# Kernel tuning notes

Hardware: AMD Instinct MI355X
Metric: run time of the kernel (lower is better)

## Reference

```python
import math
import jax, jax.numpy as jnp
import numpy as np

D_MODEL = 1024
N_HEAD = 16
HEAD_DIM = D_MODEL // N_HEAD  # 64
B = 8
L = 512
USE_GAUSSIAN = True
SCALE = 1.0  # scale=False in __init__


def rel_sin_pos_embed(seq_len, dim):
    # RelativeSinusoidalPositionalEmbedding: table row at index (pos+origin_shift)
    # holds [sin(pos*inv_freq), cos(pos*inv_freq)]; forward selects positions
    # arange(-L/2, round(L/2)) -> for even L this is -L/2 .. L/2-1.
    half = dim // 2
    inv_freq = jnp.exp(jnp.arange(half, dtype=jnp.float32) * (-math.log(10000.0) / (half - 1)))
    rel = jnp.arange(-(seq_len // 2), seq_len - seq_len // 2, dtype=jnp.float32)  # [L]
    ang = rel[:, None] * inv_freq[None, :]  # [L, half]
    return jnp.concatenate([jnp.sin(ang), jnp.cos(ang)], axis=-1)  # [L, dim]


def setup_inputs() -> dict:
    key = jax.random.key(0)
    ks = jax.random.split(key, 8)
    x = jax.random.normal(ks[0], (B, L, D_MODEL), dtype=jnp.float32)
    mask = jax.random.randint(ks[1], (B, L), 0, 2, dtype=jnp.int32)
    # guarantee at least one valid key per row so softmax never sees all -inf
    mask = mask.at[:, 0].set(1)
    qmask = jax.random.randint(ks[2], (B, L), 0, 2, dtype=jnp.int64)
    s = 0.02
    W_qkv = jax.random.normal(ks[3], (5 * D_MODEL, D_MODEL), dtype=jnp.float32) * s
    W_pos = jax.random.normal(ks[4], (3 * D_MODEL, HEAD_DIM), dtype=jnp.float32) * s
    W_fc = jax.random.normal(ks[5], (D_MODEL, D_MODEL), dtype=jnp.float32) * s
    b_fc = jnp.zeros((D_MODEL,), dtype=jnp.float32)
    # shift = abs(randn)+eps (positive), bias = -abs(randn); small scale keeps softmax sane
    shift = jnp.abs(jax.random.normal(ks[6], (1,), dtype=jnp.float32)) * 1e-4 + 1e-5
    bias = -jnp.abs(jax.random.normal(ks[7], (1,), dtype=jnp.float32))
    return {"x": x, "mask": mask, "qmask": qmask, "W_qkv": W_qkv, "W_pos": W_pos,
            "W_fc": W_fc, "b_fc": b_fc, "shift": shift, "bias": bias}


def reference(x, mask, qmask, W_qkv, W_pos, W_fc, b_fc, shift, bias):
    Bs, Ls, D = x.shape
    H, hd = N_HEAD, D // N_HEAD

    qkv = jnp.einsum('bld,ed->ble', x, W_qkv)  # [B, L, 5D]
    q, k, k1, k2, v = jnp.split(qkv, 5, axis=-1)

    def heads(t):  # [B, L, D] -> [B, H, L, hd]
        return t.reshape(Bs, Ls, H, hd).transpose(0, 2, 1, 3)

    q, k1, k2, v = heads(q), heads(k1), heads(k2), heads(v)

    pe = jax.lax.stop_gradient(rel_sin_pos_embed(Ls, hd))  # [L, hd], detached in torch
    y = jnp.einsum('ld,ed->le', pe, W_pos)  # [L, 3D]
    q_p, k1_p, k2_p = jnp.split(y, 3, axis=-1)
    q_p = q_p.reshape(Ls, H, hd).transpose(1, 0, 2)   # [H, L, hd]
    k1_p = k1_p.reshape(Ls, H, hd).transpose(1, 0, 2)  # [H, L, hd]
    k2_p = k2_p.reshape(Ls, H, hd).transpose(1, 0, 2)

    attn_self = jnp.einsum('bhid,bhjd->bhij', q, k1) + jnp.einsum('hid,hjd->hij', q_p, k1_p)[None]
    attn_others = jnp.einsum('bhid,bhjd->bhij', q, k2) + jnp.einsum('hid,hjd->hij', q_p, k2_p)[None]

    same = (qmask[:, :, None] == qmask[:, None, :])[:, None]  # [B, 1, L, L]
    attn = jnp.where(same, attn_self, 0.0) + jnp.where(same, 0.0, attn_others)
    attn = attn / SCALE
    attn = jnp.where(mask[:, None, None, :] == 0, -jnp.inf, attn)

    if USE_GAUSSIAN:
        idx = jnp.arange(Ls, dtype=jnp.float32)
        sq_dist = (idx[:, None] - idx[None, :]) ** 2  # [L, L]
        attn = attn + (-(shift[0] * sq_dist + bias[0]))[None, None]

    attn = jax.nn.softmax(attn, axis=-1)
    out = jnp.einsum('bhij,bhjd->bhid', attn, v)  # [B, H, L, hd]
    out = out.transpose(0, 2, 1, 3).reshape(Bs, Ls, D)
    return jnp.einsum('bld,ed->ble', out, W_fc) + b_fc
```

## Files before the change

### kernel.cpp

```cpp
#include <hip/hip_runtime.h>

#define DM 1024
#define HN 16
#define HD 64
#define BB 8
#define LL 512

typedef __bf16 bf16x8 __attribute__((ext_vector_type(8)));
typedef __bf16 bf16x4 __attribute__((ext_vector_type(4)));
typedef float  f32x4  __attribute__((ext_vector_type(4)));

__device__ __forceinline__ void cvt8(const float* __restrict__ in,
                                     __bf16* __restrict__ out, int i) {
    const float4* p = (const float4*)in + (size_t)i * 2;
    float4 a = p[0], b = p[1];
    bf16x8 v;
    v[0] = (__bf16)a.x; v[1] = (__bf16)a.y; v[2] = (__bf16)a.z; v[3] = (__bf16)a.w;
    v[4] = (__bf16)b.x; v[5] = (__bf16)b.y; v[6] = (__bf16)b.z; v[7] = (__bf16)b.w;
    ((bf16x8*)out)[i] = v;
}

__global__ __launch_bounds__(512) void prep_kernel(
    const int* __restrict__ qmask, const int* __restrict__ maskp,
    const float* __restrict__ x, const float* __restrict__ W_qkv,
    const float* __restrict__ W_pos, const float* __restrict__ W_fc,
    int* __restrict__ perm, int* __restrict__ pmask, float* __restrict__ posf,
    int* __restrict__ nzA, __bf16* __restrict__ PEb, __bf16* __restrict__ Wposb,
    __bf16* __restrict__ Wfcb, __bf16* __restrict__ Xb, __bf16* __restrict__ Wqkvb)
{
    const int blk = blockIdx.x, tid = threadIdx.x;
    if (blk < 8) {
        int b = blk, i = tid;
        int qm = qmask[b * LL + i];
        unsigned long long bz = __ballot(qm == 0);
        int wid = i >> 6, lane = i & 63;
        __shared__ int wz[8];
        int pzw = __popcll(bz & ((1ULL << lane) - 1ULL));
        if (lane == 0) wz[wid] = __popcll(bz);
        __syncthreads();
        int base = 0, nz = 0;
#pragma unroll
        for (int w2 = 0; w2 < 8; ++w2) { int c = wz[w2]; if (w2 < wid) base += c; nz += c; }
        int zbefore = base + pzw;
        int pos = (qm == 0) ? zbefore : (nz + (i - zbefore));
        perm[b * LL + pos] = i;
        pmask[b * LL + pos] = maskp[b * LL + i];
        posf[b * LL + pos] = (float)i;
        if (i == 0) nzA[b] = nz;
    } else if (blk < 72) {
        int idx = (blk - 8) * 512 + tid;
        int l = idx >> 6, d = idx & 63;
        float p = (float)(l - LL / 2);
        const float cexp = -9.210340371976184f / 31.0f;
        float val;
        if (d < 32) { float f = expf((float)d * cexp);        val = sinf(p * f); }
        else        { float f = expf((float)(d - 32) * cexp); val = cosf(p * f); }
        PEb[idx] = (__bf16)val;
    } else if (blk < 120) {
        cvt8(W_pos, Wposb, (blk - 72) * 512 + tid);
    } else if (blk < 376) {
        cvt8(W_fc, Wfcb, (blk - 120) * 512 + tid);
    } else if (blk < 1400) {
        cvt8(x, Xb, (blk - 376) * 512 + tid);
    } else if (blk < 1656) {
        cvt8(W_qkv, Wqkvb, (blk - 1400) * 512 + tid);
    } else {
        cvt8(W_qkv + 2097152, Wqkvb + 1048576, (blk - 1656) * 512 + tid);
    }
}

template<int MODE>
__global__ __launch_bounds__(256, 4) void gemm_mfma(
    const __bf16* __restrict__ A, const __bf16* __restrict__ Bm,
    __bf16* __restrict__ Qc, __bf16* __restrict__ K1c,
    __bf16* __restrict__ K2c, __bf16* __restrict__ Vn,
    float* __restrict__ outF, const float* __restrict__ bias, int K)
{
    __shared__ __bf16 smem[128 * 136];
    __bf16* As = smem;
    __bf16* Bs = smem + 8192;
    __bf16* Cs = smem;
    const int tid = threadIdx.x;
    const int lane = tid & 63;
    const int w = tid >> 6;
    const int wm = w >> 1, wn = w & 1;
    const int n0 = blockIdx.x * 128;
    const int m0 = blockIdx.y * 128;
    const int fr = lane & 15;
    const int fq = lane >> 4;

    const int srow = tid >> 3;
    const int scol = (tid & 7) ^ (srow & 7);
    const __bf16* Ag = A + (size_t)(m0 + srow) * K + scol * 8;
    const __bf16* Bg = Bm + (size_t)(n0 + srow) * K + scol * 8;
    char* AsB = (char*)As + (size_t)w * 1024;
    char* BsB = (char*)Bs + (size_t)w * 1024;

    f32x4 acc[4][4] = {};

    for (int k0 = 0; k0 < K; k0 += 64) {
#pragma unroll
        for (int r = 0; r < 4; ++r) {
            __builtin_amdgcn_global_load_lds(Ag + k0 + (size_t)(r * 32) * K, AsB + r * 4096, 16, 0, 0);
            __builtin_amdgcn_global_load_lds(Bg + k0 + (size_t)(r * 32) * K, BsB + r * 4096, 16, 0, 0);
        }
        __syncthreads();

#pragma unroll
        for (int kk = 0; kk < 2; ++kk) {
            const int so = ((kk * 4 + fq) ^ (fr & 7)) * 8;
            bf16x8 af[4], bfr[4];
#pragma unroll
            for (int i = 0; i < 4; ++i)
                af[i] = *(const bf16x8*)(As + (size_t)(wm * 64 + i * 16 + fr) * 64 + so);
#pragma unroll
            for (int j = 0; j < 4; ++j)
                bfr[j] = *(const bf16x8*)(Bs + (size_t)(wn * 64 + j * 16 + fr) * 64 + so);
#pragma unroll
            for (int i = 0; i < 4; ++i)
#pragma unroll
                for (int j = 0; j < 4; ++j)
                    acc[i][j] = __builtin_amdgcn_mfma_f32_16x16x32_bf16(bfr[j], af[i], acc[i][j], 0, 0, 0);
        }
        __syncthreads();
    }

    if constexpr (MODE == 0 || MODE == 2) {
#pragma unroll
        for (int i = 0; i < 4; ++i) {
            int mloc = wm * 64 + i * 16 + fr;
#pragma unroll
            for (int j = 0; j < 4; ++j) {
                int nloc = wn * 64 + j * 16 + fq * 4;
                bf16x4 v;
#pragma unroll
                for (int r = 0; r < 4; ++r) v[r] = (__bf16)acc[i][j][r];
                *(bf16x4*)(Cs + (size_t)mloc * 136 + nloc) = v;
            }
        }
        __syncthreads();
        if constexpr (MODE == 0) {
            const int c = n0 >> 10;
            __bf16* T = (c == 0) ? Qc : (c == 1) ? K1c : (c == 2) ? K2c : Vn;
            const int b = m0 >> 9, l0 = m0 & 511, h0 = (n0 >> 6) & 15;
#pragma unroll
            for (int rnd = 0; rnd < 8; ++rnd) {
                int Ci = rnd * 256 + tid;
                int m = Ci >> 4, nch = Ci & 15;
                bf16x8 v = *(const bf16x8*)(Cs + (size_t)m * 136 + nch * 8);
                int hl = nch >> 3, d = (nch & 7) * 8;
                size_t bh2 = (size_t)(b * HN + h0 + hl);
                if (c < 3) *(bf16x8*)(T + (bh2 * LL + l0 + m) * 128 + d) = v;
                else       *(bf16x8*)(T + (bh2 * LL + l0 + m) * 64  + d) = v;
            }
        } else {
            const int c = n0 >> 10;
            __bf16* T = (c == 0) ? Qc : (c == 1) ? K1c : K2c;
#pragma unroll
            for (int rnd = 0; rnd < 8; ++rnd) {
                int Ci = rnd * 256 + tid;
                int m = Ci >> 4, nch = Ci & 15;
                bf16x8 v = *(const bf16x8*)(Cs + (size_t)m * 136 + nch * 8);
                int eg = n0 + nch * 8;
                int h = (eg >> 6) & 15, d = eg & 63;
                size_t off = ((size_t)h * LL + (m0 + m)) * 128 + 64 + d;
#pragma unroll
                for (int b = 0; b < 8; ++b)
                    *(bf16x8*)(T + (size_t)b * (HN * LL * 128) + off) = v;
            }
        }
    } else {
#pragma unroll
        for (int i = 0; i < 4; ++i) {
            int m = m0 + wm * 64 + i * 16 + fr;
#pragma unroll
            for (int j = 0; j < 4; ++j) {
                int nn = n0 + wn * 64 + j * 16 + fq * 4;
                float4 bv = *(const float4*)(bias + nn);
                *(float4*)(outF + (size_t)m * DM + nn) =
                    make_float4(acc[i][j][0] + bv.x, acc[i][j][1] + bv.y,
                                acc[i][j][2] + bv.z, acc[i][j][3] + bv.w);
            }
        }
    }
}

__global__ __launch_bounds__(256) void vtrans_kernel(const __bf16* __restrict__ Vn,
                                                     const int* __restrict__ perm,
                                                     __bf16* __restrict__ Vt) {
    __shared__ __bf16 Ts[64][72];
    int bh = blockIdx.x >> 3, lt = blockIdx.x & 7;
    int b = bh >> 4;
    int r = threadIdx.x >> 2, s = threadIdx.x & 3;
    int orow = perm[b * LL + lt * 64 + r];
    const __bf16* src = Vn + ((size_t)bh * LL + orow) * 64;
    *(bf16x8*)&Ts[r][s * 16]     = *(const bf16x8*)(src + s * 16);
    *(bf16x8*)&Ts[r][s * 16 + 8] = *(const bf16x8*)(src + s * 16 + 8);
    __syncthreads();
    __bf16* dst = Vt + ((size_t)bh * 64 + r) * LL + lt * 64 + s * 16;
    bf16x8 a, bvv;
#pragma unroll
    for (int e = 0; e < 8; ++e) { a[e] = Ts[s * 16 + e][r]; bvv[e] = Ts[s * 16 + 8 + e][r]; }
    *(bf16x8*)dst = a;
    *(bf16x8*)(dst + 8) = bvv;
}

__global__ __launch_bounds__(512, 2) void attn_kernel(
    const __bf16* __restrict__ Qc, const __bf16* __restrict__ K1c,
    const __bf16* __restrict__ K2c, const __bf16* __restrict__ Vt,
    const int* __restrict__ pmask, const int* __restrict__ perm,
    const float* __restrict__ posf, const int* __restrict__ nzA,
    const float* __restrict__ shiftp, const float* __restrict__ biasp,
    __bf16* __restrict__ AO)
{
    __shared__ __bf16 Ke[2][64 * 128];
    __shared__ __bf16 Vts[64 * 72];
    __shared__ __bf16 Sb[8 * 16 * 40];
    __shared__ __align__(16) float posL[64];

    const int tid = threadIdx.x;
    const int lane = tid & 63;
    const int wid = tid >> 6;
    const int fr = lane & 15;
    const int fq = lane >> 4;
    const int fx = fr & 7;

    const int bid = (blockIdx.x & 7) * 64 + (blockIdx.x >> 3);
    const int qt = bid & 3;
    const int h  = (bid >> 2) & 15;
    const int b  = bid >> 6;
    const size_t bh = (size_t)(b * HN + h);
    const int nz = nzA[b];
    const int q0blk = qt * 128;
    const int s = q0blk + wid * 16 + fr;
    const int pi = perm[b * LL + s];
    const bool need0 = (q0blk < nz);
    const bool need1 = (q0blk + 127 >= nz);
    const int w0 = q0blk + wid * 16;
    const bool wneed0 = (w0 < nz);
    const bool wneed1 = (w0 + 15 >= nz);
    const int qmI = (s >= nz) ? 1 : 0;

    const float sft = shiftp[0];

    int co[4];
#pragma unroll
    for (int kf = 0; kf < 4; ++kf) co[kf] = ((kf * 4 + fq) ^ fx) * 8;

    bf16x8 qf[4];
    {
        const __bf16* qrow = Qc + (bh * LL + pi) * 128;
#pragma unroll
        for (int kf = 0; kf < 4; ++kf)
            qf[kf] = *(const bf16x8*)(qrow + kf * 32 + fq * 8);
    }

    float mrun = -1e30f, lrun = 0.f;
    f32x4 ot[4] = {};
    const float qposf = (float)pi;

    const __bf16* K1g0 = K1c + bh * LL * 128;
    const __bf16* K2g0 = K2c + bh * LL * 128;
    const __bf16* Vtg0 = Vt + bh * 64 * LL;
    __bf16* Sw = Sb + wid * 16 * 40;

    const int krr = tid >> 4;
    const int ku  = tid & 15;
    const int vrr = tid >> 3;
    const int vu  = tid & 7;

    bf16x8 rk0[2], rk1[2], rv;
    int pm; float ppos;

#define LOAD_TILE(tt)                                                              \
    {                                                                              \
        int j0_ = (tt) * 64;                                                       \
        _Pragma("unroll")                                                          \
        for (int p = 0; p < 2; ++p) {                                              \
            int sr = j0_ + p * 32 + krr;                                           \
            int orow = perm[b * LL + sr];                                          \
            int qmj = (sr >= nz) ? 1 : 0;                                          \
            const __bf16* s1 = (qmj ? K2g0 : K1g0) + (size_t)orow * 128 + ku * 8;  \
            const __bf16* s2 = (qmj ? K1g0 : K2g0) + (size_t)orow * 128 + ku * 8;  \
            if (need0) rk0[p] = *(const bf16x8*)s1;                                \
            if (need1) rk1[p] = *(const bf16x8*)s2;                                \
        }                                                                          \
        rv = *(const bf16x8*)(Vtg0 + (size_t)vrr * LL + j0_ + vu * 8);             \
        pm = pmask[b * LL + j0_ + lane];                                           \
        ppos = posf[b * LL + j0_ + lane];                                          \
    }

    LOAD_TILE(0);

    for (int t = 0; t < 8; ++t) {
        __syncthreads();
        {
#pragma unroll
            for (int p = 0; p < 2; ++p) {
                int rr = p * 32 + krr;
                int sc = (ku ^ (rr & 7)) * 8;
                if (need0) *(bf16x8*)(Ke[0] + rr * 128 + sc) = rk0[p];
                if (need1) *(bf16x8*)(Ke[1] + rr * 128 + sc) = rk1[p];
            }
            *(bf16x8*)(Vts + vrr * 72 + vu * 8) = rv;
            if (wid == 0) posL[lane] = ppos;
        }
        unsigned long long kbits = __ballot(pm != 0);
        if (t < 7) LOAD_TILE(t + 1);
        __syncthreads();

        f32x4 acc[4];
        if (wneed0 != wneed1) {
            const __bf16* Ks = wneed0 ? Ke[0] : Ke[1];
            __builtin_amdgcn_s_setprio(1);
#pragma unroll
            for (int kb = 0; kb < 4; ++kb) {
                const __bf16* row = Ks + (kb * 16 + fr) * 128;
                bf16x8 af[4];
#pragma unroll
                for (int kf = 0; kf < 4; ++kf)
                    af[kf] = *(const bf16x8*)(row + co[kf]);
                f32x4 a = {};
#pragma unroll
                for (int kf = 0; kf < 4; ++kf)
                    a = __builtin_amdgcn_mfma_f32_16x16x32_bf16(af[kf], qf[kf], a, 0, 0, 0);
                acc[kb] = a;
            }
            __builtin_amdgcn_s_setprio(0);
        } else {
            __builtin_amdgcn_s_setprio(1);
#pragma unroll
            for (int kb = 0; kb < 4; ++kb) {
                const __bf16* r0 = Ke[0] + (kb * 16 + fr) * 128;
                const __bf16* r1 = Ke[1] + (kb * 16 + fr) * 128;
                bf16x8 a0f[4], a1f[4];
#pragma unroll
                for (int kf = 0; kf < 4; ++kf) {
                    a0f[kf] = *(const bf16x8*)(r0 + co[kf]);
                    a1f[kf] = *(const bf16x8*)(r1 + co[kf]);
                }
                f32x4 t0 = {}, t1 = {};
#pragma unroll
                for (int kf = 0; kf < 4; ++kf) {
                    t0 = __builtin_amdgcn_mfma_f32_16x16x32_bf16(a0f[kf], qf[kf], t0, 0, 0, 0);
                    t1 = __builtin_amdgcn_mfma_f32_16x16x32_bf16(a1f[kf], qf[kf], t1, 0, 0, 0);
                }
#pragma unroll
                for (int r = 0; r < 4; ++r) acc[kb][r] = qmI ? t1[r] : t0[r];
            }
            __builtin_amdgcn_s_setprio(0);
        }

#pragma unroll
        for (int kb = 0; kb < 4; ++kb) {
            f32x4 pj = *(const f32x4*)(posL + kb * 16 + fq * 4);
#pragma unroll
            for (int r = 0; r < 4; ++r) {
                float di = qposf - pj[r];
                acc[kb][r] -= sft * di * di;
            }
        }

        float lmax = acc[0][0];
#pragma unroll
        for (int kb = 0; kb < 4; ++kb)
#pragma unroll
            for (int r = 0; r < 4; ++r) lmax = fmaxf(lmax, acc[kb][r]);
        if (!__all(lmax <= mrun + 8.f)) {
            float mn = fmaxf(mrun, lmax);
            mn = fmaxf(mn, __shfl_xor(mn, 16));
            mn = fmaxf(mn, __shfl_xor(mn, 32));
            float sc = __expf(mrun - mn);
            mrun = mn;
            lrun *= sc;
#pragma unroll
            for (int fd = 0; fd < 4; ++fd)
#pragma unroll
                for (int r = 0; r < 4; ++r) ot[fd][r] *= sc;
        }
        float sum = 0.f;
#pragma unroll
        for (int kb = 0; kb < 4; ++kb)
#pragma unroll
            for (int r = 0; r < 4; ++r) {
                int ko = kb * 16 + fq * 4 + r;
                float p = ((int)(kbits >> ko) & 1) ? __expf(acc[kb][r] - mrun) : 0.f;
                acc[kb][r] = p;
                sum += p;
            }
        sum += __shfl_xor(sum, 16);
        sum += __shfl_xor(sum, 32);
        lrun += sum;

        __builtin_amdgcn_s_setprio(1);
#pragma unroll
        for (int half = 0; half < 2; ++half) {
#pragma unroll
            for (int kk = 0; kk < 2; ++kk) {
                int kb = half * 2 + kk;
                bf16x4 pk;
#pragma unroll
                for (int r = 0; r < 4; ++r) pk[r] = (__bf16)acc[kb][r];
                *(bf16x4*)(Sw + fr * 40 + kk * 16 + fq * 4) = pk;
            }
            bf16x8 pf = *(const bf16x8*)(Sw + fr * 40 + fq * 8);
#pragma unroll
            for (int fd = 0; fd < 4; ++fd) {
                bf16x8 vf = *(const bf16x8*)(Vts + (fd * 16 + fr) * 72 + half * 32 + fq * 8);
                ot[fd] = __builtin_amdgcn_mfma_f32_16x16x32_bf16(vf, pf, ot[fd], 0, 0, 0);
            }
        }
        __builtin_amdgcn_s_setprio(0);
    }
#undef LOAD_TILE

    __syncthreads();
    {
        const float inv = 1.0f / lrun;
        __bf16* Ew = Ke[0] + (size_t)(wid * 16) * 72;
#pragma unroll
        for (int fd = 0; fd < 4; ++fd) {
            bf16x4 o;
#pragma unroll
            for (int r = 0; r < 4; ++r) o[r] = (__bf16)(ot[fd][r] * inv);
            *(bf16x4*)(Ew + fr * 72 + fd * 16 + fq * 4) = o;
        }
    }
    __syncthreads();
    {
        int r = tid >> 2, c = tid & 3;
        int pir = perm[b * LL + q0blk + r];
        const __bf16* src = Ke[0] + (size_t)r * 72;
        __bf16* dst = AO + ((size_t)(b * LL + pir)) * DM + h * 64;
        *(bf16x8*)(dst + c * 8)      = *(const bf16x8*)(src + c * 8);
        *(bf16x8*)(dst + 32 + c * 8) = *(const bf16x8*)(src + 32 + c * 8);
    }
}

extern "C" void kernel_launch(void* const* d_in, const int* in_sizes, int n_in,
                              void* d_out, int out_size, void* d_ws, size_t ws_size,
                              hipStream_t stream) {
    const float* x     = (const float*)d_in[0];
    const int*   mask  = (const int*)d_in[1];
    const int*   qmask = (const int*)d_in[2];
    const float* W_qkv = (const float*)d_in[3];
    const float* W_pos = (const float*)d_in[4];
    const float* W_fc  = (const float*)d_in[5];
    const float* b_fc  = (const float*)d_in[6];
    const float* shift = (const float*)d_in[7];
    const float* bias  = (const float*)d_in[8];
    float* out = (float*)d_out;

    __bf16* Qcb  = (__bf16*)d_ws;
    __bf16* K1cb = Qcb  + 8388608;
    __bf16* K2cb = K1cb + 8388608;
    __bf16* Vnb  = K2cb + 8388608;
    __bf16* Vtb  = Vnb  + 4194304;
    __bf16* Xb   = Vtb  + 4194304;
    __bf16* Wqkvb = Xb  + 4194304;
    __bf16* AOb   = Xb;
    __bf16* PEb   = Wqkvb + 4194304;
    __bf16* Wposb = PEb + 32768;
    __bf16* Wfcb  = Wposb + 196608;
    int* permA = (int*)(Wfcb + 1048576);
    int* nzA   = permA + 4096;
    int* pmaskA = nzA + 8;
    float* posfA = (float*)(pmaskA + 4096);

    prep_kernel<<<2424, 512, 0, stream>>>(qmask, mask, x, W_qkv, W_pos, W_fc,
                                          permA, pmaskA, posfA, nzA,
                                          PEb, Wposb, Wfcb, Xb, Wqkvb);
    gemm_mfma<0><<<dim3(32, 32), 256, 0, stream>>>(Xb, Wqkvb, Qcb, K1cb, K2cb, Vnb,
                                                   nullptr, nullptr, 1024);
    vtrans_kernel<<<1024, 256, 0, stream>>>(Vnb, permA, Vtb);
    gemm_mfma<2><<<dim3(24, 4), 256, 0, stream>>>(PEb, Wposb, Qcb, K1cb, K2cb, nullptr,
                                                  nullptr, nullptr, 64);
    attn_kernel<<<512, 512, 0, stream>>>(Qcb, K1cb, K2cb, Vtb, pmaskA, permA,
                                         posfA, nzA, shift, bias, AOb);
    gemm_mfma<1><<<dim3(8, 32), 256, 0, stream>>>(AOb, Wfcb, nullptr, nullptr, nullptr,
                                                  nullptr, out, b_fc, 1024);
}
```

Baseline: 132.2 us.

## Schedule mixed-group attention tiles first and use 128-key tiles for pure tiles

The prep kernel now builds a schedule table that launches, for each (batch, head), the query tile straddling the qmask boundary first and the single-key-set tiles afterwards. This is longest-job-first ordering, meant to cut tail imbalance across the grid. Tiles that need only one of K1/K2 take a new path that stages 128 keys per iteration into the freed second K buffer, halving the loop trips and barriers. Mixed tiles keep the old 64-key path. The cost is a wider V smem tile, more registers in the 8-block score loop, and extra code size.

```diff
diff --git a/kernel.cpp b/kernel.cpp
--- a/kernel.cpp
+++ b/kernel.cpp
@@ -25,7 +25,8 @@
     const float* __restrict__ x, const float* __restrict__ W_qkv,
     const float* __restrict__ W_pos, const float* __restrict__ W_fc,
     int* __restrict__ perm, int* __restrict__ pmask, float* __restrict__ posf,
-    int* __restrict__ nzA, __bf16* __restrict__ PEb, __bf16* __restrict__ Wposb,
+    int* __restrict__ nzA, int* __restrict__ sched,
+    __bf16* __restrict__ PEb, __bf16* __restrict__ Wposb,
     __bf16* __restrict__ Wfcb, __bf16* __restrict__ Xb, __bf16* __restrict__ Wqkvb)
 {
     const int blk = blockIdx.x, tid = threadIdx.x;
@@ -47,6 +48,18 @@
         pmask[b * LL + pos] = maskp[b * LL + i];
         posf[b * LL + pos] = (float)i;
         if (i == 0) nzA[b] = nz;
+        if (i < 16) {
+            int bh2 = b * 16 + i;
+            int g = i & 7;
+            int idx = b * 2 + (i >> 3);
+            int qtm = nz >> 7; if (qtm > 3) qtm = 3;
+            sched[idx * 8 + g] = (bh2 << 2) | qtm;
+#pragma unroll
+            for (int j = 0; j < 3; ++j) {
+                int qtj = j + (j >= qtm ? 1 : 0);
+                sched[(16 + idx * 3 + j) * 8 + g] = (bh2 << 2) | qtj;
+            }
+        }
     } else if (blk < 72) {
         int idx = (blk - 8) * 512 + tid;
         int l = idx >> 6, d = idx & 63;
@@ -210,13 +223,13 @@
     const __bf16* __restrict__ K2c, const __bf16* __restrict__ Vt,
     const int* __restrict__ pmask, const int* __restrict__ perm,
     const float* __restrict__ posf, const int* __restrict__ nzA,
-    const float* __restrict__ shiftp, const float* __restrict__ biasp,
-    __bf16* __restrict__ AO)
+    const int* __restrict__ sched,
+    const float* __restrict__ shiftp, __bf16* __restrict__ AO)
 {
     __shared__ __bf16 Ke[2][64 * 128];
-    __shared__ __bf16 Vts[64 * 72];
+    __shared__ __bf16 Vts[64 * 136];
     __shared__ __bf16 Sb[8 * 16 * 40];
-    __shared__ __align__(16) float posL[64];
+    __shared__ __align__(16) float posL[128];
 
     const int tid = threadIdx.x;
     const int lane = tid & 63;
@@ -225,10 +238,11 @@
     const int fq = lane >> 4;
     const int fx = fr & 7;
 
-    const int bid = (blockIdx.x & 7) * 64 + (blockIdx.x >> 3);
-    const int qt = bid & 3;
-    const int h  = (bid >> 2) & 15;
-    const int b  = bid >> 6;
+    const int e = sched[blockIdx.x];
+    const int qt = e & 3;
+    const int bh_i = e >> 2;
+    const int h = bh_i & 15;
+    const int b = bh_i >> 4;
     const size_t bh = (size_t)(b * HN + h);
     const int nz = nzA[b];
     const int q0blk = qt * 128;
@@ -263,59 +277,59 @@
     const __bf16* K2g0 = K2c + bh * LL * 128;
     const __bf16* Vtg0 = Vt + bh * 64 * LL;
     __bf16* Sw = Sb + wid * 16 * 40;
+    __bf16* KeF = &Ke[0][0];
 
     const int krr = tid >> 4;
     const int ku  = tid & 15;
     const int vrr = tid >> 3;
     const int vu  = tid & 7;
 
-    bf16x8 rk0[2], rk1[2], rv;
-    int pm; float ppos;
-
-#define LOAD_TILE(tt)                                                              \
-    {                                                                              \
-        int j0_ = (tt) * 64;                                                       \
-        _Pragma("unroll")                                                          \
-        for (int p = 0; p < 2; ++p) {                                              \
-            int sr = j0_ + p * 32 + krr;                                           \
-            int orow = perm[b * LL + sr];                                          \
-            int qmj = (sr >= nz) ? 1 : 0;                                          \
-            const __bf16* s1 = (qmj ? K2g0 : K1g0) + (size_t)orow * 128 + ku * 8;  \
-            const __bf16* s2 = (qmj ? K1g0 : K2g0) + (size_t)orow * 128 + ku * 8;  \
-            if (need0) rk0[p] = *(const bf16x8*)s1;                                \
-            if (need1) rk1[p] = *(const bf16x8*)s2;                                \
-        }                                                                          \
-        rv = *(const bf16x8*)(Vtg0 + (size_t)vrr * LL + j0_ + vu * 8);             \
-        pm = pmask[b * LL + j0_ + lane];                                           \
-        ppos = posf[b * LL + j0_ + lane];                                          \
-    }
-
-    LOAD_TILE(0);
-
-    for (int t = 0; t < 8; ++t) {
-        __syncthreads();
-        {
-#pragma unroll
-            for (int p = 0; p < 2; ++p) {
+    if (!(need0 && need1)) {
+        const __bf16* KA = need0 ? K1g0 : K2g0;
+        const __bf16* KB = need0 ? K2g0 : K1g0;
+        bf16x8 rkP[4], rvP[2];
+        int pm0, pm1; float ppos;
+
+#define LOADP(tt)                                                                   \
+    {                                                                               \
+        int j0_ = (tt) * 128;                                                       \
+        _Pragma("unroll")                                                           \
+        for (int p = 0; p < 4; ++p) {                                               \
+            int sr = j0_ + p * 32 + krr;                                            \
+            int orow = perm[b * LL + sr];                                           \
+            const __bf16* srcp = ((sr >= nz) ? KB : KA) + (size_t)orow * 128 + ku * 8; \
+            rkP[p] = *(const bf16x8*)srcp;                                          \
+        }                                                                           \
+        _Pragma("unroll")                                                           \
+        for (int p = 0; p < 2; ++p)                                                 \
+            rvP[p] = *(const bf16x8*)(Vtg0 + (size_t)vrr * LL + j0_ + (vu + 8 * p) * 8); \
+        pm0 = pmask[b * LL + j0_ + lane];                                           \
+        pm1 = pmask[b * LL + j0_ + 64 + lane];                                      \
+        ppos = posf[b * LL + j0_ + (tid & 127)];                                    \
+    }
+
+        LOADP(0);
+        for (int t = 0; t < 4; ++t) {
+            __syncthreads();
+#pragma unroll
+            for (int p = 0; p < 4; ++p) {
                 int rr = p * 32 + krr;
-                int sc = (ku ^ (rr & 7)) * 8;
-                if (need0) *(bf16x8*)(Ke[0] + rr * 128 + sc) = rk0[p];
-                if (need1) *(bf16x8*)(Ke[1] + rr * 128 + sc) = rk1[p];
-            }
-            *(bf16x8*)(Vts + vrr * 72 + vu * 8) = rv;
-            if (wid == 0) posL[lane] = ppos;
-        }
-        unsigned long long kbits = __ballot(pm != 0);
-        if (t < 7) LOAD_TILE(t + 1);
-        __syncthreads();
-
-        f32x4 acc[4];
-        if (wneed0 != wneed1) {
-            const __bf16* Ks = wneed0 ? Ke[0] : Ke[1];
+                *(bf16x8*)(KeF + rr * 128 + (ku ^ (rr & 7)) * 8) = rkP[p];
+            }
+#pragma unroll
+            for (int p = 0; p < 2; ++p)
+                *(bf16x8*)(Vts + vrr * 136 + (vu + 8 * p) * 8) = rvP[p];
+            if (tid < 128) posL[tid] = ppos;
+            unsigned long long m0b = __ballot(pm0 != 0);
+            unsigned long long m1b = __ballot(pm1 != 0);
+            if (t < 3) LOADP(t + 1);
+            __syncthreads();
+
+            f32x4 acc[8];
             __builtin_amdgcn_s_setprio(1);
 #pragma unroll
-            for (int kb = 0; kb < 4; ++kb) {
-                const __bf16* row = Ks + (kb * 16 + fr) * 128;
+            for (int kb = 0; kb < 8; ++kb) {
+                const __bf16* row = KeF + (kb * 16 + fr) * 128;
                 bf16x8 af[4];
 #pragma unroll
                 for (int kf = 0; kf < 4; ++kf)
@@ -327,97 +341,220 @@
                 acc[kb] = a;
             }
             __builtin_amdgcn_s_setprio(0);
-        } else {
+
+#pragma unroll
+            for (int kb = 0; kb < 8; ++kb) {
+                f32x4 pj = *(const f32x4*)(posL + kb * 16 + fq * 4);
+#pragma unroll
+                for (int r = 0; r < 4; ++r) {
+                    float di = qposf - pj[r];
+                    acc[kb][r] -= sft * di * di;
+                }
+            }
+
+            float lmax = acc[0][0];
+#pragma unroll
+            for (int kb = 0; kb < 8; ++kb)
+#pragma unroll
+                for (int r = 0; r < 4; ++r) lmax = fmaxf(lmax, acc[kb][r]);
+            if (!__all(lmax <= mrun + 8.f)) {
+                float mn = fmaxf(mrun, lmax);
+                mn = fmaxf(mn, __shfl_xor(mn, 16));
+                mn = fmaxf(mn, __shfl_xor(mn, 32));
+                float sc = __expf(mrun - mn);
+                mrun = mn;
+                lrun *= sc;
+#pragma unroll
+                for (int fd = 0; fd < 4; ++fd)
+#pragma unroll
+                    for (int r = 0; r < 4; ++r) ot[fd][r] *= sc;
+            }
+            float sum = 0.f;
+#pragma unroll
+            for (int kb = 0; kb < 8; ++kb)
+#pragma unroll
+                for (int r = 0; r < 4; ++r) {
+                    int ko = (kb & 3) * 16 + fq * 4 + r;
+                    unsigned long long mb = (kb < 4) ? m0b : m1b;
+                    float p = ((int)(mb >> ko) & 1) ? __expf(acc[kb][r] - mrun) : 0.f;
+                    acc[kb][r] = p;
+                    sum += p;
+                }
+            sum += __shfl_xor(sum, 16);
+            sum += __shfl_xor(sum, 32);
+            lrun += sum;
+
             __builtin_amdgcn_s_setprio(1);
 #pragma unroll
+            for (int qtr = 0; qtr < 4; ++qtr) {
+#pragma unroll
+                for (int kk = 0; kk < 2; ++kk) {
+                    int kb = qtr * 2 + kk;
+                    bf16x4 pk;
+#pragma unroll
+                    for (int r = 0; r < 4; ++r) pk[r] = (__bf16)acc[kb][r];
+                    *(bf16x4*)(Sw + fr * 40 + kk * 16 + fq * 4) = pk;
+                }
+                bf16x8 pf = *(const bf16x8*)(Sw + fr * 40 + fq * 8);
+#pragma unroll
+                for (int fd = 0; fd < 4; ++fd) {
+                    bf16x8 vf = *(const bf16x8*)(Vts + (fd * 16 + fr) * 136 + qtr * 32 + fq * 8);
+                    ot[fd] = __builtin_amdgcn_mfma_f32_16x16x32_bf16(vf, pf, ot[fd], 0, 0, 0);
+                }
+            }
+            __builtin_amdgcn_s_setprio(0);
+        }
+#undef LOADP
+    } else {
+        bf16x8 rk0[2], rk1[2], rv;
+        int pm; float ppos;
+
+#define LOADM(tt)                                                                   \
+    {                                                                               \
+        int j0_ = (tt) * 64;                                                        \
+        _Pragma("unroll")                                                           \
+        for (int p = 0; p < 2; ++p) {                                               \
+            int sr = j0_ + p * 32 + krr;                                            \
+            int orow = perm[b * LL + sr];                                           \
+            int qmj = (sr >= nz) ? 1 : 0;                                           \
+            const __bf16* s1 = (qmj ? K2g0 : K1g0) + (size_t)orow * 128 + ku * 8;   \
+            const __bf16* s2 = (qmj ? K1g0 : K2g0) + (size_t)orow * 128 + ku * 8;   \
+            rk0[p] = *(const bf16x8*)s1;                                            \
+            rk1[p] = *(const bf16x8*)s2;                                            \
+        }                                                                           \
+        rv = *(const bf16x8*)(Vtg0 + (size_t)vrr * LL + j0_ + vu * 8);              \
+        pm = pmask[b * LL + j0_ + lane];                                            \
+        ppos = posf[b * LL + j0_ + lane];                                           \
+    }
+
+        LOADM(0);
+        for (int t = 0; t < 8; ++t) {
+            __syncthreads();
+            {
+#pragma unroll
+                for (int p = 0; p < 2; ++p) {
+                    int rr = p * 32 + krr;
+                    int sc = (ku ^ (rr & 7)) * 8;
+                    *(bf16x8*)(KeF + rr * 128 + sc) = rk0[p];
+                    *(bf16x8*)(KeF + 8192 + rr * 128 + sc) = rk1[p];
+                }
+                *(bf16x8*)(Vts + vrr * 136 + vu * 8) = rv;
+                if (wid == 0) posL[lane] = ppos;
+            }
+            unsigned long long kbits = __ballot(pm != 0);
+            if (t < 7) LOADM(t + 1);
+            __syncthreads();
+
+            f32x4 acc[4];
+            if (wneed0 != wneed1) {
+                const __bf16* Ks = wneed0 ? KeF : (KeF + 8192);
+                __builtin_amdgcn_s_setprio(1);
+#pragma unroll
+                for (int kb = 0; kb < 4; ++kb) {
+                    const __bf16* row = Ks + (kb * 16 + fr) * 128;
+                    bf16x8 af[4];
+#pragma unroll
+                    for (int kf = 0; kf < 4; ++kf)
+                        af[kf] = *(const bf16x8*)(row + co[kf]);
+                    f32x4 a = {};
+#pragma unroll
+                    for (int kf = 0; kf < 4; ++kf)
+                        a = __builtin_amdgcn_mfma_f32_16x16x32_bf16(af[kf], qf[kf], a, 0, 0, 0);
+                    acc[kb] = a;
+                }
+                __builtin_amdgcn_s_setprio(0);
+            } else {
+                __builtin_amdgcn_s_setprio(1);
+#pragma unroll
+                for (int kb = 0; kb < 4; ++kb) {
+                    const __bf16* r0 = KeF + (kb * 16 + fr) * 128;
+                    const __bf16* r1 = KeF + 8192 + (kb * 16 + fr) * 128;
+                    bf16x8 a0f[4], a1f[4];
+#pragma unroll
+                    for (int kf = 0; kf < 4; ++kf) {
+                        a0f[kf] = *(const bf16x8*)(r0 + co[kf]);
+                        a1f[kf] = *(const bf16x8*)(r1 + co[kf]);
+                    }
+                    f32x4 t0 = {}, t1 = {};
+#pragma unroll
+                    for (int kf = 0; kf < 4; ++kf) {
+                        t0 = __builtin_amdgcn_mfma_f32_16x16x32_bf16(a0f[kf], qf[kf], t0, 0, 0, 0);
+                        t1 = __builtin_amdgcn_mfma_f32_16x16x32_bf16(a1f[kf], qf[kf], t1, 0, 0, 0);
+                    }
+#pragma unroll
+                    for (int r = 0; r < 4; ++r) acc[kb][r] = qmI ? t1[r] : t0[r];
+                }
+                __builtin_amdgcn_s_setprio(0);
+            }
+
+#pragma unroll
             for (int kb = 0; kb < 4; ++kb) {
-                const __bf16* r0 = Ke[0] + (kb * 16 + fr) * 128;
-                const __bf16* r1 = Ke[1] + (kb * 16 + fr) * 128;
-                bf16x8 a0f[4], a1f[4];
-#pragma unroll
-                for (int kf = 0; kf < 4; ++kf) {
-                    a0f[kf] = *(const bf16x8*)(r0 + co[kf]);
-                    a1f[kf] = *(const bf16x8*)(r1 + co[kf]);
-                }
-                f32x4 t0 = {}, t1 = {};
-#pragma unroll
-                for (int kf = 0; kf < 4; ++kf) {
-                    t0 = __builtin_amdgcn_mfma_f32_16x16x32_bf16(a0f[kf], qf[kf], t0, 0, 0, 0);
-                    t1 = __builtin_amdgcn_mfma_f32_16x16x32_bf16(a1f[kf], qf[kf], t1, 0, 0, 0);
-                }
-#pragma unroll
-                for (int r = 0; r < 4; ++r) acc[kb][r] = qmI ? t1[r] : t0[r];
+                f32x4 pj = *(const f32x4*)(posL + kb * 16 + fq * 4);
+#pragma unroll
+                for (int r = 0; r < 4; ++r) {
+                    float di = qposf - pj[r];
+                    acc[kb][r] -= sft * di * di;
+                }
+            }
+
+            float lmax = acc[0][0];
+#pragma unroll
+            for (int kb = 0; kb < 4; ++kb)
+#pragma unroll
+                for (int r = 0; r < 4; ++r) lmax = fmaxf(lmax, acc[kb][r]);
+            if (!__all(lmax <= mrun + 8.f)) {
+                float mn = fmaxf(mrun, lmax);
+                mn = fmaxf(mn, __shfl_xor(mn, 16));
+                mn = fmaxf(mn, __shfl_xor(mn, 32));
+                float sc = __expf(mrun - mn);
+                mrun = mn;
+                lrun *= sc;
+#pragma unroll
+                for (int fd = 0; fd < 4; ++fd)
+#pragma unroll
+                    for (int r = 0; r < 4; ++r) ot[fd][r] *= sc;
+            }
+            float sum = 0.f;
+#pragma unroll
+            for (int kb = 0; kb < 4; ++kb)
+#pragma unroll
+                for (int r = 0; r < 4; ++r) {
+                    int ko = kb * 16 + fq * 4 + r;
+                    float p = ((int)(kbits >> ko) & 1) ? __expf(acc[kb][r] - mrun) : 0.f;
+                    acc[kb][r] = p;
+                    sum += p;
+                }
+            sum += __shfl_xor(sum, 16);
+            sum += __shfl_xor(sum, 32);
+            lrun += sum;
+
+            __builtin_amdgcn_s_setprio(1);
+#pragma unroll
+            for (int half = 0; half < 2; ++half) {
+#pragma unroll
+                for (int kk = 0; kk < 2; ++kk) {
+                    int kb = half * 2 + kk;
+                    bf16x4 pk;
+#pragma unroll
+                    for (int r = 0; r < 4; ++r) pk[r] = (__bf16)acc[kb][r];
+                    *(bf16x4*)(Sw + fr * 40 + kk * 16 + fq * 4) = pk;
+                }
+                bf16x8 pf = *(const bf16x8*)(Sw + fr * 40 + fq * 8);
+#pragma unroll
+                for (int fd = 0; fd < 4; ++fd) {
+                    bf16x8 vf = *(const bf16x8*)(Vts + (fd * 16 + fr) * 136 + half * 32 + fq * 8);
+                    ot[fd] = __builtin_amdgcn_mfma_f32_16x16x32_bf16(vf, pf, ot[fd], 0, 0, 0);
+                }
             }
             __builtin_amdgcn_s_setprio(0);
         }
-
-#pragma unroll
-        for (int kb = 0; kb < 4; ++kb) {
-            f32x4 pj = *(const f32x4*)(posL + kb * 16 + fq * 4);
-#pragma unroll
-            for (int r = 0; r < 4; ++r) {
-                float di = qposf - pj[r];
-                acc[kb][r] -= sft * di * di;
-            }
-        }
-
-        float lmax = acc[0][0];
-#pragma unroll
-        for (int kb = 0; kb < 4; ++kb)
-#pragma unroll
-            for (int r = 0; r < 4; ++r) lmax = fmaxf(lmax, acc[kb][r]);
-        if (!__all(lmax <= mrun + 8.f)) {
-            float mn = fmaxf(mrun, lmax);
-            mn = fmaxf(mn, __shfl_xor(mn, 16));
-            mn = fmaxf(mn, __shfl_xor(mn, 32));
-            float sc = __expf(mrun - mn);
-            mrun = mn;
-            lrun *= sc;
-#pragma unroll
-            for (int fd = 0; fd < 4; ++fd)
-#pragma unroll
-                for (int r = 0; r < 4; ++r) ot[fd][r] *= sc;
-        }
-        float sum = 0.f;
-#pragma unroll
-        for (int kb = 0; kb < 4; ++kb)
-#pragma unroll
-            for (int r = 0; r < 4; ++r) {
-                int ko = kb * 16 + fq * 4 + r;
-                float p = ((int)(kbits >> ko) & 1) ? __expf(acc[kb][r] - mrun) : 0.f;
-                acc[kb][r] = p;
-                sum += p;
-            }
-        sum += __shfl_xor(sum, 16);
-        sum += __shfl_xor(sum, 32);
-        lrun += sum;
-
-        __builtin_amdgcn_s_setprio(1);
-#pragma unroll
-        for (int half = 0; half < 2; ++half) {
-#pragma unroll
-            for (int kk = 0; kk < 2; ++kk) {
-                int kb = half * 2 + kk;
-                bf16x4 pk;
-#pragma unroll
-                for (int r = 0; r < 4; ++r) pk[r] = (__bf16)acc[kb][r];
-                *(bf16x4*)(Sw + fr * 40 + kk * 16 + fq * 4) = pk;
-            }
-            bf16x8 pf = *(const bf16x8*)(Sw + fr * 40 + fq * 8);
-#pragma unroll
-            for (int fd = 0; fd < 4; ++fd) {
-                bf16x8 vf = *(const bf16x8*)(Vts + (fd * 16 + fr) * 72 + half * 32 + fq * 8);
-                ot[fd] = __builtin_amdgcn_mfma_f32_16x16x32_bf16(vf, pf, ot[fd], 0, 0, 0);
-            }
-        }
-        __builtin_amdgcn_s_setprio(0);
-    }
-#undef LOAD_TILE
+#undef LOADM
+    }
 
     __syncthreads();
     {
         const float inv = 1.0f / lrun;
-        __bf16* Ew = Ke[0] + (size_t)(wid * 16) * 72;
+        __bf16* Ew = KeF + (size_t)(wid * 16) * 72;
 #pragma unroll
         for (int fd = 0; fd < 4; ++fd) {
             bf16x4 o;
@@ -430,7 +567,7 @@
     {
         int r = tid >> 2, c = tid & 3;
         int pir = perm[b * LL + q0blk + r];
-        const __bf16* src = Ke[0] + (size_t)r * 72;
+        const __bf16* src = KeF + (size_t)r * 72;
         __bf16* dst = AO + ((size_t)(b * LL + pir)) * DM + h * 64;
         *(bf16x8*)(dst + c * 8)      = *(const bf16x8*)(src + c * 8);
         *(bf16x8*)(dst + 32 + c * 8) = *(const bf16x8*)(src + 32 + c * 8);
@@ -466,9 +603,10 @@
     int* nzA   = permA + 4096;
     int* pmaskA = nzA + 8;
     float* posfA = (float*)(pmaskA + 4096);
+    int* schedA = (int*)(posfA + 4096);
 
     prep_kernel<<<2424, 512, 0, stream>>>(qmask, mask, x, W_qkv, W_pos, W_fc,
-                                          permA, pmaskA, posfA, nzA,
+                                          permA, pmaskA, posfA, nzA, schedA,
                                           PEb, Wposb, Wfcb, Xb, Wqkvb);
     gemm_mfma<0><<<dim3(32, 32), 256, 0, stream>>>(Xb, Wqkvb, Qcb, K1cb, K2cb, Vnb,
                                                    nullptr, nullptr, 1024);
@@ -476,7 +614,7 @@
     gemm_mfma<2><<<dim3(24, 4), 256, 0, stream>>>(PEb, Wposb, Qcb, K1cb, K2cb, nullptr,
                                                   nullptr, nullptr, 64);
     attn_kernel<<<512, 512, 0, stream>>>(Qcb, K1cb, K2cb, Vtb, pmaskA, permA,
-                                         posfA, nzA, shift, bias, AOb);
+                                         posfA, nzA, schedA, shift, AOb);
     gemm_mfma<1><<<dim3(8, 32), 256, 0, stream>>>(AOb, Wfcb, nullptr, nullptr, nullptr,
                                                   nullptr, out, b_fc, 1024);
 }
```

Result: faster. 128.0 us (-3.1%).
